# Performance work log

Hardware: AMD Instinct MI355X
Metric: run time of the kernel (lower is better)

Reference implementation:

```python
import jax, jax.numpy as jnp
import numpy as np

N, E, H, S, F = 50000, 800000, 96, 48, 24


def _mlp(x, W1, b1, W2, b2):
    # equinox MLP depth=1: Linear -> relu -> Linear (identity final activation)
    h = jax.nn.relu(x @ W1.T + b1)
    return h @ W2.T + b2


def _segment_softmax(scores, seg, num_segments):
    mx = jax.ops.segment_max(scores, seg, num_segments=num_segments)
    e = jnp.exp(scores - mx[seg])
    s = jax.ops.segment_sum(e, seg, num_segments=num_segments)
    return e / (s[seg] + 1e-9)


def setup_inputs() -> dict:
    key = jax.random.key(0)
    ks = jax.random.split(key, 32)
    def p(i, shape):
        return jax.random.normal(ks[i], shape, dtype=jnp.float32) * 0.05
    in_attn = 2 * H + 2 * S + F   # 312
    w_attn = 2 * H                # 192
    gin = 3 * H                   # 288
    inp = {
        "x": p(0, (N, H)),
        "x_s": p(1, (N, S)),
        "edge_features": p(2, (E, F)),
        "edge_index": jax.random.randint(ks[3], (2, E), 0, N),
        # fwd attention MLP: in_attn -> w_attn -> 1
        "fwd_W1": p(4, (w_attn, in_attn)), "fwd_b1": p(5, (w_attn,)),
        "fwd_W2": p(6, (1, w_attn)), "fwd_b2": p(7, (1,)),
        # rev gate MLP: in_attn -> w_attn -> 1
        "rev_W1": p(8, (w_attn, in_attn)), "rev_b1": p(9, (w_attn,)),
        "rev_W2": p(10, (1, w_attn)), "rev_b2": p(11, (1,)),
        # reset gate MLP: 3H -> 3H -> H
        "reset_W1": p(12, (gin, gin)), "reset_b1": p(13, (gin,)),
        "reset_W2": p(14, (H, gin)), "reset_b2": p(15, (H,)),
        # update gate MLP: 3H -> 3H -> H
        "update_W1": p(16, (gin, gin)), "update_b1": p(17, (gin,)),
        "update_W2": p(18, (H, gin)), "update_b2": p(19, (H,)),
        # candidate MLP: 3H -> 3H -> H
        "cand_W1": p(20, (gin, gin)), "cand_b1": p(21, (gin,)),
        "cand_W2": p(22, (H, gin)), "cand_b2": p(23, (H,)),
    }
    return inp


def reference(x, x_s, edge_features, edge_index,
              fwd_W1, fwd_b1, fwd_W2, fwd_b2,
              rev_W1, rev_b1, rev_W2, rev_b2,
              reset_W1, reset_b1, reset_W2, reset_b2,
              update_W1, update_b1, update_W2, update_b2,
              cand_W1, cand_b1, cand_W2, cand_b2):
    num_nodes = x.shape[0]
    src, dest = edge_index[0], edge_index[1]

    def compute_messages(s, d, W1, b1, W2, b2, use_softmax):
        feat = jnp.concatenate([x[s], x[d], x_s[s], x_s[d], edge_features], axis=-1)
        raw = _mlp(feat, W1, b1, W2, b2)[:, 0]  # [E]
        if use_softmax:
            raw = jax.nn.leaky_relu(raw) / jnp.sqrt(jnp.asarray(x.shape[-1], dtype=x.dtype))
            w = _segment_softmax(raw, d, num_nodes)
        else:
            w = jax.nn.sigmoid(raw)
        agg = jax.ops.segment_sum(x[s] * w[:, None], d, num_segments=num_nodes)
        return agg, w

    fwd_msgs, fwd_w = compute_messages(src, dest, fwd_W1, fwd_b1, fwd_W2, fwd_b2, True)
    rev_msgs, rev_w = compute_messages(dest, src, rev_W1, rev_b1, rev_W2, rev_b2, False)

    messages = jnp.concatenate([fwd_msgs, rev_msgs], axis=-1)  # [N, 2H]
    gate_input = jnp.concatenate([x, messages], axis=-1)        # [N, 3H]
    r_gate = jax.nn.sigmoid(_mlp(gate_input, reset_W1, reset_b1, reset_W2, reset_b2))
    z_gate = jax.nn.sigmoid(_mlp(gate_input, update_W1, update_b1, update_W2, update_b2))
    cand_input = jnp.concatenate([r_gate * x, messages], axis=-1)
    candidate = jnp.tanh(_mlp(cand_input, cand_W1, cand_b1, cand_W2, cand_b2))
    update = (1 - z_gate) * x + z_gate * candidate
    return (update, fwd_w, rev_w, z_gate, r_gate)
```

## Files before the change

### kernel.cpp

```cpp
#include <hip/hip_runtime.h>
#include <math.h>

typedef unsigned short u16;
typedef unsigned int   u32;

#define HDIM 96
#define SDIM 48
#define FDIM 24
#define KA   312
#define WATT 192
#define KG   288

#define AS_E  328
#define KT_A  10
#define KT_G  9
#define NS    296

#define NFRAG (2 * KT_A * 12 * 64)
#define W1F_Q (KT_G * 18 * 64)
#define W2F_Q (KT_G * 6 * 64)
#define NODEF_Q (3 * (W1F_Q + W2F_Q))

typedef __attribute__((ext_vector_type(8))) __bf16 bf16x8;
typedef __attribute__((ext_vector_type(4))) float  f32x4;

__device__ __forceinline__ u16 f2bf(float f) {
  u32 u = __float_as_uint(f);
  u = (u + 0x7FFFu + ((u >> 16) & 1u)) >> 16;
  return (u16)u;
}
__device__ __forceinline__ float bf2f(u16 v) {
  return __uint_as_float((u32)v << 16);
}
__device__ __forceinline__ u32 pack2(float a, float b) {
  return (u32)f2bf(a) | ((u32)f2bf(b) << 16);
}
__device__ __forceinline__ f32x4 mfma_bf16(bf16x8 a, bf16x8 b, f32x4 c) {
  return __builtin_amdgcn_mfma_f32_16x16x32_bf16(a, b, c, 0, 0, 0);
}

__global__ __launch_bounds__(256) void w_prep(
    const float* __restrict__ fW1, const float* __restrict__ rW1,
    uint4* __restrict__ Bfrag)
{
  const int idx = blockIdx.x * 256 + threadIdx.x;
  if (idx >= NFRAG) return;
  const int lane = idx & 63;
  const int frag = idx >> 6;
  const int nt   = frag % 12;
  const int rest = frag / 12;
  const int kt   = rest % KT_A;
  const int mlp  = rest / KT_A;
  const int q = lane >> 4, c = lane & 15;
  const int n  = nt * 16 + c;
  const int p0 = kt * 16 + q * 4;
  const float* W = mlp ? rW1 : fW1;
  u32 v[4];
#pragma unroll
  for (int w = 0; w < 4; ++w) {
    const int p = p0 + w;
    u32 val = 0u;
    if (p < 156) {
      int src = p;
      if (mlp) {
        if (src < 48)       src += 48;
        else if (src < 96)  src -= 48;
        else if (src < 120) src += 24;
        else if (src < 144) src -= 24;
      }
      const float2 wv = *(const float2*)(W + (size_t)n * KA + 2 * src);
      val = pack2(wv.x, wv.y);
    }
    v[w] = val;
  }
  Bfrag[idx] = make_uint4(v[0], v[1], v[2], v[3]);
}

__global__ __launch_bounds__(256) void w_prep_node(
    const float* __restrict__ W, uint4* __restrict__ outf, int NT)
{
  const int nfrag = KT_G * NT * 64;
  const int idx = blockIdx.x * 256 + threadIdx.x;
  if (idx >= nfrag) return;
  const int lane = idx & 63;
  const int frag = idx >> 6;
  const int nt = frag % NT, kt = frag / NT;
  const int q = lane >> 4, c = lane & 15;
  const int n = nt * 16 + c;
  const int k0 = kt * 32 + q * 8;
  u32 v[4];
#pragma unroll
  for (int w = 0; w < 4; ++w) {
    const float2 wv = *(const float2*)(W + (size_t)n * KG + k0 + 2 * w);
    v[w] = pack2(wv.x, wv.y);
  }
  outf[idx] = make_uint4(v[0], v[1], v[2], v[3]);
}

__global__ __launch_bounds__(256) void x_prep(
    const float* __restrict__ x, const float* __restrict__ xs,
    u32* __restrict__ xb, u32* __restrict__ xsb, int N)
{
  const int i = blockIdx.x * 256 + threadIdx.x;
  const int nx = N * 48;
  if (i < nx) {
    const float2 v = ((const float2*)x)[i];
    xb[i] = pack2(v.x, v.y);
  } else if (i < nx + N * 24) {
    const float2 v = ((const float2*)xs)[i - nx];
    xsb[i - nx] = pack2(v.x, v.y);
  }
}

__global__ __launch_bounds__(256, 2) void edge_kernel(
    const u32* __restrict__ xb, const u32* __restrict__ xsb,
    const float* __restrict__ ef, const int* __restrict__ ei,
    const u16* __restrict__ Bfrag,
    const float* __restrict__ fb1, const float* __restrict__ fW2,
    const float* __restrict__ fb2,
    const float* __restrict__ rb1, const float* __restrict__ rW2,
    const float* __restrict__ rb2,
    float* __restrict__ pe, float* __restrict__ out_revw, int N, int E)
{
  __shared__ __align__(16) u16 Alds[64 * AS_E];
  __shared__ float red[4][64];

  const int tid  = threadIdx.x;
  const int wave = tid >> 6, lane = tid & 63;
  const int q = lane >> 4, c = lane & 15;
  const int e0 = blockIdx.x * 64;

  {
    u32* Aw = (u32*)Alds;
    const int el = tid >> 2, sub = tid & 3;
    const int e = min(e0 + el, E - 1);
    int s = ei[e], d = ei[(size_t)E + e];
    s = min(max(s, 0), N - 1); d = min(max(d, 0), N - 1);
    const u32* xs_ = xb  + (size_t)s * 48;
    const u32* xd_ = xb  + (size_t)d * 48;
    const u32* ss_ = xsb + (size_t)s * 24;
    const u32* sd_ = xsb + (size_t)d * 24;
    for (int p = sub; p < 160; p += 4) {
      u32 v = 0u;
      if (p < 48)       v = xs_[p];
      else if (p < 96)  v = xd_[p - 48];
      else if (p < 120) v = ss_[p - 96];
      else if (p < 144) v = sd_[p - 120];
      else if (p < 156) {
        const float2 w = *(const float2*)(ef + (size_t)e * 24 + 2 * (p - 144));
        v = pack2(w.x, w.y);
      }
      Aw[el * (AS_E / 2) + p] = v;
    }
  }
  __syncthreads();

  const bf16x8* __restrict__ Bf = (const bf16x8*)Bfrag;

  for (int mlp = 0; mlp < 2; ++mlp) {
    f32x4 acc[4][3];
#pragma unroll
    for (int m = 0; m < 4; ++m)
      for (int t = 0; t < 3; ++t)
        acc[m][t] = (f32x4){0.f, 0.f, 0.f, 0.f};

#pragma unroll
    for (int kt = 0; kt < KT_A; ++kt) {
      bf16x8 a[4];
#pragma unroll
      for (int m = 0; m < 4; ++m)
        a[m] = *(const bf16x8*)&Alds[(m * 16 + c) * AS_E + kt * 32 + q * 8];
#pragma unroll
      for (int t = 0; t < 3; ++t) {
        const bf16x8 b =
            Bf[(((mlp * KT_A + kt) * 12) + wave * 3 + t) * 64 + lane];
#pragma unroll
        for (int m = 0; m < 4; ++m)
          acc[m][t] = mfma_bf16(a[m], b, acc[m][t]);
      }
    }

    const float* b1p = mlp ? rb1 : fb1;
    const float* W2p = mlp ? rW2 : fW2;
    float p[4][4];
#pragma unroll
    for (int m = 0; m < 4; ++m)
      for (int r = 0; r < 4; ++r) p[m][r] = 0.f;
#pragma unroll
    for (int t = 0; t < 3; ++t) {
      const int n = (wave * 3 + t) * 16 + c;
      const float b1f = b1p[n];
      const float w2f = W2p[n];
#pragma unroll
      for (int m = 0; m < 4; ++m)
        for (int r = 0; r < 4; ++r) {
          float h = acc[m][t][r] + b1f;
          h = h > 0.f ? h : 0.f;
          p[m][r] += h * w2f;
        }
    }
    for (int off = 1; off <= 8; off <<= 1)
#pragma unroll
      for (int m = 0; m < 4; ++m)
        for (int r = 0; r < 4; ++r)
          p[m][r] += __shfl_xor(p[m][r], off, 64);

    __syncthreads();
    if (c == 0) {
#pragma unroll
      for (int m = 0; m < 4; ++m)
        for (int r = 0; r < 4; ++r)
          red[wave][m * 16 + q * 4 + r] = p[m][r];
    }
    __syncthreads();

    if (tid < 64 && e0 + tid < E) {
      float raw = red[0][tid] + red[1][tid] + red[2][tid] + red[3][tid];
      const int e = e0 + tid;
      if (mlp == 0) {
        raw += fb2[0];
        const float lr = raw > 0.f ? raw : 0.01f * raw;
        pe[e] = __expf(lr * 0.10206207261596575f);
      } else {
        raw += rb2[0];
        out_revw[e] = 1.f / (1.f + __expf(-raw));
      }
    }
  }
}

__global__ __launch_bounds__(256) void k_hist(
    const int* __restrict__ ei, int* __restrict__ deg_d,
    int* __restrict__ deg_s, int N, int E)
{
  const int e = blockIdx.x * 256 + threadIdx.x;
  if (e >= E) return;
  const int s = min(max(ei[e], 0), N - 1);
  const int d = min(max(ei[(size_t)E + e], 0), N - 1);
  atomicAdd(&deg_d[d], 1);
  atomicAdd(&deg_s[s], 1);
}

__global__ __launch_bounds__(256) void k_scan1(
    const int* __restrict__ deg_d, const int* __restrict__ deg_s,
    int* __restrict__ start_d, int* __restrict__ start_s,
    int* __restrict__ bsum_d, int* __restrict__ bsum_s, int N)
{
  __shared__ int sh[256];
  const int t = threadIdx.x, i = blockIdx.x * 256 + t;
  {
    const int v = (i < N) ? deg_d[i] : 0;
    sh[t] = v; __syncthreads();
    for (int off = 1; off < 256; off <<= 1) {
      const int u = (t >= off) ? sh[t - off] : 0;
      __syncthreads();
      sh[t] += u;
      __syncthreads();
    }
    if (i < N) start_d[i] = sh[t] - v;
    if (t == 255) bsum_d[blockIdx.x] = sh[255];
    __syncthreads();
  }
  {
    const int v = (i < N) ? deg_s[i] : 0;
    sh[t] = v; __syncthreads();
    for (int off = 1; off < 256; off <<= 1) {
      const int u = (t >= off) ? sh[t - off] : 0;
      __syncthreads();
      sh[t] += u;
      __syncthreads();
    }
    if (i < N) start_s[i] = sh[t] - v;
    if (t == 255) bsum_s[blockIdx.x] = sh[255];
  }
}

__global__ void k_scan2(int* bsum_d, int* bsum_s, int nb) {
  if (threadIdx.x == 0) {
    int r = 0;
    for (int b = 0; b < nb; ++b) { const int t = bsum_d[b]; bsum_d[b] = r; r += t; }
  } else if (threadIdx.x == 1) {
    int r = 0;
    for (int b = 0; b < nb; ++b) { const int t = bsum_s[b]; bsum_s[b] = r; r += t; }
  }
}

__global__ __launch_bounds__(256) void k_scan3(
    int* __restrict__ start_d, int* __restrict__ start_s,
    const int* __restrict__ bsum_d, const int* __restrict__ bsum_s,
    int* __restrict__ pos_d, int* __restrict__ pos_s, int N)
{
  const int i = blockIdx.x * 256 + threadIdx.x;
  if (i >= N) return;
  const int b = i >> 8;
  const int vd = start_d[i] + bsum_d[b]; start_d[i] = vd; pos_d[i] = vd;
  const int vs = start_s[i] + bsum_s[b]; start_s[i] = vs; pos_s[i] = vs;
}

__global__ __launch_bounds__(256) void k_fill(
    const int* __restrict__ ei, int* __restrict__ pos_d,
    int* __restrict__ pos_s, int* __restrict__ eidx_d,
    int* __restrict__ eidx_s, int N, int E)
{
  const int e = blockIdx.x * 256 + threadIdx.x;
  if (e >= E) return;
  const int s = min(max(ei[e], 0), N - 1);
  const int d = min(max(ei[(size_t)E + e], 0), N - 1);
  eidx_d[atomicAdd(&pos_d[d], 1)] = e;
  eidx_s[atomicAdd(&pos_s[s], 1)] = e;
}

template <int DIR>
__global__ __launch_bounds__(256) void k_agg(
    const float* __restrict__ x, const int* __restrict__ ei,
    const float* __restrict__ pe, const float* __restrict__ revw,
    const int* __restrict__ start, const int* __restrict__ endp,
    const int* __restrict__ eidx,
    u16* __restrict__ outm, float* __restrict__ out_fwdw, int N, int E)
{
  const int g = threadIdx.x >> 5;
  const int l = threadIdx.x & 31;
  const int n = blockIdx.x * 8 + g;
  if (n >= N) return;
  const int beg = start[n], end = endp[n];

  float inv = 1.f;
  if (DIR == 0) {
    float sum = 0.f;
    for (int i = beg + l; i < end; i += 32) sum += pe[eidx[i]];
    for (int off = 16; off; off >>= 1) sum += __shfl_xor(sum, off, 32);
    inv = 1.f / (sum + 1e-9f);
    for (int i = beg + l; i < end; i += 32) {
      const int e = eidx[i];
      out_fwdw[e] = pe[e] * inv;
    }
  }

  float a0 = 0.f, a1 = 0.f, a2 = 0.f;
  for (int i = beg; i < end; ++i) {
    const int e = eidx[i];
    const float w = (DIR == 0) ? pe[e] * inv : revw[e];
    const int o = (DIR == 0) ? min(max(ei[e], 0), N - 1)
                             : min(max(ei[(size_t)E + e], 0), N - 1);
    const float* xr = x + (size_t)o * 96;
    a0 += w * xr[l];
    a1 += w * xr[l + 32];
    a2 += w * xr[l + 64];
  }
  u16* orow = outm + (size_t)n * 96;
  orow[l] = f2bf(a0); orow[l + 32] = f2bf(a1); orow[l + 64] = f2bf(a2);
}

__device__ __forceinline__ void node_mlp(
    const u16* __restrict__ Alds, u16* __restrict__ Hlds,
    const bf16x8* __restrict__ W1f, const bf16x8* __restrict__ W2f,
    const float* __restrict__ b1,
    int wave, int lane, int q, int c, int ntc, int ntc2,
    f32x4 (&acc2)[2][2])
{
  f32x4 acc[2][5];
#pragma unroll
  for (int m = 0; m < 2; ++m)
    for (int t = 0; t < 5; ++t) acc[m][t] = (f32x4){0.f, 0.f, 0.f, 0.f};

#pragma unroll
  for (int kt = 0; kt < KT_G; ++kt) {
    const bf16x8 a0 = *(const bf16x8*)&Alds[c * NS + kt * 32 + q * 8];
    const bf16x8 a1 = *(const bf16x8*)&Alds[(16 + c) * NS + kt * 32 + q * 8];
#pragma unroll
    for (int t = 0; t < 5; ++t) {
      if (t < ntc) {
        const int nt = wave + 4 * t;
        const bf16x8 b = W1f[(kt * 18 + nt) * 64 + lane];
        acc[0][t] = mfma_bf16(a0, b, acc[0][t]);
        acc[1][t] = mfma_bf16(a1, b, acc[1][t]);
      }
    }
  }

  __syncthreads();
#pragma unroll
  for (int t = 0; t < 5; ++t) {
    if (t < ntc) {
      const int n = (wave + 4 * t) * 16 + c;
      const float b1f = b1[n];
#pragma unroll
      for (int m = 0; m < 2; ++m)
        for (int r = 0; r < 4; ++r) {
          float h = acc[m][t][r] + b1f;
          h = h > 0.f ? h : 0.f;
          Hlds[(m * 16 + q * 4 + r) * NS + n] = f2bf(h);
        }
    }
  }
  __syncthreads();

#pragma unroll
  for (int m = 0; m < 2; ++m)
    for (int t = 0; t < 2; ++t) acc2[m][t] = (f32x4){0.f, 0.f, 0.f, 0.f};
#pragma unroll
  for (int kt = 0; kt < KT_G; ++kt) {
    const bf16x8 a0 = *(const bf16x8*)&Hlds[c * NS + kt * 32 + q * 8];
    const bf16x8 a1 = *(const bf16x8*)&Hlds[(16 + c) * NS + kt * 32 + q * 8];
#pragma unroll
    for (int t = 0; t < 2; ++t) {
      if (t < ntc2) {
        const int nt = wave + 4 * t;
        const bf16x8 b = W2f[(kt * 6 + nt) * 64 + lane];
        acc2[0][t] = mfma_bf16(a0, b, acc2[0][t]);
        acc2[1][t] = mfma_bf16(a1, b, acc2[1][t]);
      }
    }
  }
}

__global__ __launch_bounds__(256) void node_fused(
    const float* __restrict__ x, const u32* __restrict__ xb,
    const u32* __restrict__ fwdmb, const u32* __restrict__ revmb,
    const uint4* __restrict__ NodeF,
    const float* __restrict__ b1r, const float* __restrict__ b2r,
    const float* __restrict__ b1u, const float* __restrict__ b2u,
    const float* __restrict__ b1c, const float* __restrict__ b2c,
    float* __restrict__ out_r, float* __restrict__ out_z,
    float* __restrict__ out_upd, int N)
{
  __shared__ __align__(16) u16 Alds[32 * NS];
  __shared__ __align__(16) u16 Hlds[32 * NS];

  const int tid = threadIdx.x;
  const int wave = tid >> 6, lane = tid & 63;
  const int q = lane >> 4, c = lane & 15;
  const int n0 = blockIdx.x * 32;
  const int ntc  = (wave < 2) ? 5 : 4;
  const int ntc2 = (wave < 2) ? 2 : 1;

  {
    u32* Aw = (u32*)Alds;
    const int nl = tid >> 3, sub = tid & 7;
    const int node = min(n0 + nl, N - 1);
    const u32* xr = xb    + (size_t)node * 48;
    const u32* fr = fwdmb + (size_t)node * 48;
    const u32* rr = revmb + (size_t)node * 48;
    for (int p = sub; p < 144; p += 8) {
      u32 v;
      if (p < 48)      v = xr[p];
      else if (p < 96) v = fr[p - 48];
      else             v = rr[p - 96];
      Aw[nl * (NS / 2) + p] = v;
    }
  }
  __syncthreads();

  const bf16x8* W1fr = (const bf16x8*)(NodeF);
  const bf16x8* W2fr = (const bf16x8*)(NodeF + W1F_Q);
  const bf16x8* W1fu = (const bf16x8*)(NodeF + W1F_Q + W2F_Q);
  const bf16x8* W2fu = (const bf16x8*)(NodeF + 2 * W1F_Q + W2F_Q);
  const bf16x8* W1fc = (const bf16x8*)(NodeF + 2 * (W1F_Q + W2F_Q));
  const bf16x8* W2fc = (const bf16x8*)(NodeF + 3 * W1F_Q + 2 * W2F_Q);

  f32x4 acc2[2][2];

  node_mlp(Alds, Hlds, W1fr, W2fr, b1r, wave, lane, q, c, ntc, ntc2, acc2);
  float r_reg[2][2][4];
#pragma unroll
  for (int t = 0; t < 2; ++t) {
    if (t < ntc2) {
      const int n2 = (wave + 4 * t) * 16 + c;
      const float b2f = b2r[n2];
#pragma unroll
      for (int m = 0; m < 2; ++m)
        for (int r = 0; r < 4; ++r) {
          const float v = acc2[m][t][r] + b2f;
          const float rv = 1.f / (1.f + __expf(-v));
          r_reg[t][m][r] = rv;
          const int node = n0 + m * 16 + q * 4 + r;
          if (node < N) out_r[(size_t)node * HDIM + n2] = rv;
        }
    }
  }

  node_mlp(Alds, Hlds, W1fu, W2fu, b1u, wave, lane, q, c, ntc, ntc2, acc2);
  float z_reg[2][2][4];
#pragma unroll
  for (int t = 0; t < 2; ++t) {
    if (t < ntc2) {
      const int n2 = (wave + 4 * t) * 16 + c;
      const float b2f = b2u[n2];
#pragma unroll
      for (int m = 0; m < 2; ++m)
        for (int r = 0; r < 4; ++r) {
          const float v = acc2[m][t][r] + b2f;
          const float zv = 1.f / (1.f + __expf(-v));
          z_reg[t][m][r] = zv;
          const int node = n0 + m * 16 + q * 4 + r;
          if (node < N) out_z[(size_t)node * HDIM + n2] = zv;
        }
    }
  }

#pragma unroll
  for (int t = 0; t < 2; ++t) {
    if (t < ntc2) {
      const int n2 = (wave + 4 * t) * 16 + c;
#pragma unroll
      for (int m = 0; m < 2; ++m)
        for (int r = 0; r < 4; ++r) {
          const int row = m * 16 + q * 4 + r;
          const int idx = row * NS + n2;
          Alds[idx] = f2bf(bf2f(Alds[idx]) * r_reg[t][m][r]);
        }
    }
  }
  __syncthreads();

  node_mlp(Alds, Hlds, W1fc, W2fc, b1c, wave, lane, q, c, ntc, ntc2, acc2);
#pragma unroll
  for (int t = 0; t < 2; ++t) {
    if (t < ntc2) {
      const int n2 = (wave + 4 * t) * 16 + c;
      const float b2f = b2c[n2];
#pragma unroll
      for (int m = 0; m < 2; ++m)
        for (int r = 0; r < 4; ++r) {
          const int node = n0 + m * 16 + q * 4 + r;
          if (node < N) {
            const float v = acc2[m][t][r] + b2f;
            const float ct = tanhf(v);
            const float z = z_reg[t][m][r];
            const float xv = x[(size_t)node * HDIM + n2];
            out_upd[(size_t)node * HDIM + n2] = (1.f - z) * xv + z * ct;
          }
        }
    }
  }
}

__global__ void sentinel_kernel(float* out, int n, float val) {
  const int i = blockIdx.x * 256 + threadIdx.x;
  if (i < n) out[i] = val;
}

extern "C" void kernel_launch(void* const* d_in, const int* in_sizes, int n_in,
                              void* d_out, int out_size, void* d_ws, size_t ws_size,
                              hipStream_t stream) {
  const float* x  = (const float*)d_in[0];
  const float* xs = (const float*)d_in[1];
  const float* ef = (const float*)d_in[2];
  const int*   ei = (const int*)d_in[3];

  const int N = in_sizes[0] / HDIM;
  const int E = in_sizes[3] / 2;

  float* out = (float*)d_out;

  const int NB = (N + 255) / 256;

  const bool sizes_ok =
      n_in == 24 && NB <= 1024 &&
      in_sizes[0] == N * HDIM && in_sizes[1] == N * SDIM &&
      in_sizes[2] == E * FDIM && in_sizes[3] == 2 * E &&
      in_sizes[4] == WATT * KA && in_sizes[5] == WATT &&
      in_sizes[6] == WATT && in_sizes[7] == 1 &&
      in_sizes[12] == KG * KG && in_sizes[13] == KG &&
      in_sizes[14] == HDIM * KG && in_sizes[15] == HDIM &&
      out_size == 3 * N * HDIM + 2 * E;
  if (!sizes_ok) {
    sentinel_kernel<<<(out_size + 255) / 256, 256, 0, stream>>>(out, out_size, 777.0f);
    return;
  }

  const size_t eA = ((size_t)E + 3) & ~(size_t)3;
  const size_t needed =
      (eA + (size_t)NFRAG * 4 + (size_t)NODEF_Q * 4 +
       (size_t)N * 48 + (size_t)N * 24 + 2 * (size_t)N * 48 +
       6 * (size_t)N + 2048 + 2 * (size_t)E) * 4;
  if (ws_size < needed) {
    sentinel_kernel<<<(out_size + 255) / 256, 256, 0, stream>>>(out, out_size, 12345.0f);
    return;
  }
  float* pe    = (float*)d_ws;
  uint4* Bfrag = (uint4*)((u32*)d_ws + eA);
  uint4* NodeF = Bfrag + NFRAG;
  u32*   xbw   = (u32*)(NodeF + NODEF_Q);
  u32*   xsbw  = xbw + (size_t)N * 48;
  u32*   fwdmb = xsbw + (size_t)N * 24;
  u32*   revmb = fwdmb + (size_t)N * 48;
  int* deg_d   = (int*)(revmb + (size_t)N * 48);
  int* deg_s   = deg_d + N;
  int* start_d = deg_s + N;
  int* start_s = start_d + N;
  int* pos_d   = start_s + N;
  int* pos_s   = pos_d + N;
  int* bsum_d  = pos_s + N;
  int* bsum_s  = bsum_d + 1024;
  int* eidx_d  = bsum_s + 1024;
  int* eidx_s  = eidx_d + E;

  float* out_update = out;
  float* out_fwdw   = out + (size_t)N * HDIM;
  float* out_revw   = out_fwdw + E;
  float* out_z      = out_revw + E;
  float* out_r      = out_z + (size_t)N * HDIM;

  (void)hipMemsetAsync(deg_d, 0, 2 * (size_t)N * sizeof(int), stream);

  w_prep<<<(NFRAG + 255) / 256, 256, 0, stream>>>(
      (const float*)d_in[4], (const float*)d_in[8], Bfrag);
  const int g1 = (KT_G * 18 * 64 + 255) / 256;
  const int g2 = (KT_G * 6 * 64 + 255) / 256;
  w_prep_node<<<g1, 256, 0, stream>>>((const float*)d_in[12], NodeF, 18);
  w_prep_node<<<g2, 256, 0, stream>>>((const float*)d_in[14], NodeF + W1F_Q, 6);
  w_prep_node<<<g1, 256, 0, stream>>>((const float*)d_in[16],
                                      NodeF + W1F_Q + W2F_Q, 18);
  w_prep_node<<<g2, 256, 0, stream>>>((const float*)d_in[18],
                                      NodeF + 2 * W1F_Q + W2F_Q, 6);
  w_prep_node<<<g1, 256, 0, stream>>>((const float*)d_in[20],
                                      NodeF + 2 * (W1F_Q + W2F_Q), 18);
  w_prep_node<<<g2, 256, 0, stream>>>((const float*)d_in[22],
                                      NodeF + 3 * W1F_Q + 2 * W2F_Q, 6);
  x_prep<<<(N * 72 + 255) / 256, 256, 0, stream>>>(x, xs, xbw, xsbw, N);

  const int eblk = (E + 255) / 256;
  k_hist<<<eblk, 256, 0, stream>>>(ei, deg_d, deg_s, N, E);
  k_scan1<<<NB, 256, 0, stream>>>(deg_d, deg_s, start_d, start_s,
                                  bsum_d, bsum_s, N);
  k_scan2<<<1, 64, 0, stream>>>(bsum_d, bsum_s, NB);
  k_scan3<<<NB, 256, 0, stream>>>(start_d, start_s, bsum_d, bsum_s,
                                  pos_d, pos_s, N);
  k_fill<<<eblk, 256, 0, stream>>>(ei, pos_d, pos_s, eidx_d, eidx_s, N, E);

  edge_kernel<<<(E + 63) / 64, 256, 0, stream>>>(
      xbw, xsbw, ef, ei, (const u16*)Bfrag,
      (const float*)d_in[5], (const float*)d_in[6], (const float*)d_in[7],
      (const float*)d_in[9], (const float*)d_in[10], (const float*)d_in[11],
      pe, out_revw, N, E);

  const int ablk = (N + 7) / 8;
  k_agg<0><<<ablk, 256, 0, stream>>>(x, ei, pe, out_revw, start_d, pos_d,
                                     eidx_d, (u16*)fwdmb, out_fwdw, N, E);
  k_agg<1><<<ablk, 256, 0, stream>>>(x, ei, pe, out_revw, start_s, pos_s,
                                     eidx_s, (u16*)revmb, out_fwdw, N, E);

  const int nblk = (N + 31) / 32;
  node_fused<<<nblk, 256, 0, stream>>>(
      x, xbw, fwdmb, revmb, NodeF,
      (const float*)d_in[13], (const float*)d_in[15],
      (const float*)d_in[17], (const float*)d_in[19],
      (const float*)d_in[21], (const float*)d_in[23],
      out_r, out_z, out_update, N);
}
```

Baseline: 1.164 ms.

## Vectorize gathers to 16-byte loads and double node MLP tile to 64 rows

The edge kernel's feature gather now loads 16-byte vectors per thread, each thread filling a contiguous 10-uint4 chunk of the LDS row instead of strided 4-byte loads. The node kernel goes from 32 to 64 nodes per block, so each weight fragment loaded from global memory feeds four MFMAs instead of two, roughly halving weight traffic per node. It also vectorizes its LDS fill and adds a min-blocks-per-CU hint of 2 to launch bounds. The cost is more accumulator registers and double the LDS per block, which may reduce occupancy, and half as many node blocks.

```diff
diff --git a/kernel.cpp b/kernel.cpp
--- a/kernel.cpp
+++ b/kernel.cpp
@@ -131,27 +131,42 @@
   const int e0 = blockIdx.x * 64;
 
   {
-    u32* Aw = (u32*)Alds;
     const int el = tid >> 2, sub = tid & 3;
     const int e = min(e0 + el, E - 1);
     int s = ei[e], d = ei[(size_t)E + e];
     s = min(max(s, 0), N - 1); d = min(max(d, 0), N - 1);
-    const u32* xs_ = xb  + (size_t)s * 48;
-    const u32* xd_ = xb  + (size_t)d * 48;
-    const u32* ss_ = xsb + (size_t)s * 24;
-    const u32* sd_ = xsb + (size_t)d * 24;
-    for (int p = sub; p < 160; p += 4) {
-      u32 v = 0u;
-      if (p < 48)       v = xs_[p];
-      else if (p < 96)  v = xd_[p - 48];
-      else if (p < 120) v = ss_[p - 96];
-      else if (p < 144) v = sd_[p - 120];
-      else if (p < 156) {
-        const float2 w = *(const float2*)(ef + (size_t)e * 24 + 2 * (p - 144));
-        v = pack2(w.x, w.y);
+    const uint4* xsr = (const uint4*)(xb  + (size_t)s * 48);
+    const uint4* xdr = (const uint4*)(xb  + (size_t)d * 48);
+    const uint4* ssr = (const uint4*)(xsb + (size_t)s * 24);
+    const uint4* sdr = (const uint4*)(xsb + (size_t)d * 24);
+    uint4* Arow = (uint4*)&Alds[el * AS_E];
+    uint4 v[10];
+    if (sub == 0) {
+#pragma unroll
+      for (int i = 0; i < 10; ++i) v[i] = xsr[i];
+    } else if (sub == 1) {
+      v[0] = xsr[10]; v[1] = xsr[11];
+#pragma unroll
+      for (int i = 0; i < 8; ++i) v[2 + i] = xdr[i];
+    } else if (sub == 2) {
+#pragma unroll
+      for (int i = 0; i < 4; ++i) v[i] = xdr[8 + i];
+#pragma unroll
+      for (int i = 0; i < 6; ++i) v[4 + i] = ssr[i];
+    } else {
+#pragma unroll
+      for (int i = 0; i < 6; ++i) v[i] = sdr[i];
+      const float4* efr = (const float4*)(ef + (size_t)e * 24);
+#pragma unroll
+      for (int u = 0; u < 3; ++u) {
+        const float4 a = efr[2 * u], b = efr[2 * u + 1];
+        v[6 + u] = make_uint4(pack2(a.x, a.y), pack2(a.z, a.w),
+                              pack2(b.x, b.y), pack2(b.z, b.w));
       }
-      Aw[el * (AS_E / 2) + p] = v;
-    }
+      v[9] = make_uint4(0u, 0u, 0u, 0u);
+    }
+#pragma unroll
+    for (int i = 0; i < 10; ++i) Arow[sub * 10 + i] = v[i];
   }
   __syncthreads();
 
@@ -356,24 +371,27 @@
     const bf16x8* __restrict__ W1f, const bf16x8* __restrict__ W2f,
     const float* __restrict__ b1,
     int wave, int lane, int q, int c, int ntc, int ntc2,
-    f32x4 (&acc2)[2][2])
-{
-  f32x4 acc[2][5];
-#pragma unroll
-  for (int m = 0; m < 2; ++m)
+    f32x4 (&acc2)[4][2])
+{
+  f32x4 acc[4][5];
+#pragma unroll
+  for (int m = 0; m < 4; ++m)
     for (int t = 0; t < 5; ++t) acc[m][t] = (f32x4){0.f, 0.f, 0.f, 0.f};
 
 #pragma unroll
   for (int kt = 0; kt < KT_G; ++kt) {
-    const bf16x8 a0 = *(const bf16x8*)&Alds[c * NS + kt * 32 + q * 8];
-    const bf16x8 a1 = *(const bf16x8*)&Alds[(16 + c) * NS + kt * 32 + q * 8];
+    bf16x8 a[4];
+#pragma unroll
+    for (int m = 0; m < 4; ++m)
+      a[m] = *(const bf16x8*)&Alds[(m * 16 + c) * NS + kt * 32 + q * 8];
 #pragma unroll
     for (int t = 0; t < 5; ++t) {
       if (t < ntc) {
         const int nt = wave + 4 * t;
         const bf16x8 b = W1f[(kt * 18 + nt) * 64 + lane];
-        acc[0][t] = mfma_bf16(a0, b, acc[0][t]);
-        acc[1][t] = mfma_bf16(a1, b, acc[1][t]);
+#pragma unroll
+        for (int m = 0; m < 4; ++m)
+          acc[m][t] = mfma_bf16(a[m], b, acc[m][t]);
       }
     }
   }
@@ -385,7 +403,7 @@
       const int n = (wave + 4 * t) * 16 + c;
       const float b1f = b1[n];
 #pragma unroll
-      for (int m = 0; m < 2; ++m)
+      for (int m = 0; m < 4; ++m)
         for (int r = 0; r < 4; ++r) {
           float h = acc[m][t][r] + b1f;
           h = h > 0.f ? h : 0.f;
@@ -396,25 +414,28 @@
   __syncthreads();
 
 #pragma unroll
-  for (int m = 0; m < 2; ++m)
+  for (int m = 0; m < 4; ++m)
     for (int t = 0; t < 2; ++t) acc2[m][t] = (f32x4){0.f, 0.f, 0.f, 0.f};
 #pragma unroll
   for (int kt = 0; kt < KT_G; ++kt) {
-    const bf16x8 a0 = *(const bf16x8*)&Hlds[c * NS + kt * 32 + q * 8];
-    const bf16x8 a1 = *(const bf16x8*)&Hlds[(16 + c) * NS + kt * 32 + q * 8];
+    bf16x8 a[4];
+#pragma unroll
+    for (int m = 0; m < 4; ++m)
+      a[m] = *(const bf16x8*)&Hlds[(m * 16 + c) * NS + kt * 32 + q * 8];
 #pragma unroll
     for (int t = 0; t < 2; ++t) {
       if (t < ntc2) {
         const int nt = wave + 4 * t;
         const bf16x8 b = W2f[(kt * 6 + nt) * 64 + lane];
-        acc2[0][t] = mfma_bf16(a0, b, acc2[0][t]);
-        acc2[1][t] = mfma_bf16(a1, b, acc2[1][t]);
+#pragma unroll
+        for (int m = 0; m < 4; ++m)
+          acc2[m][t] = mfma_bf16(a[m], b, acc2[m][t]);
       }
     }
   }
 }
 
-__global__ __launch_bounds__(256) void node_fused(
+__global__ __launch_bounds__(256, 2) void node_fused(
     const float* __restrict__ x, const u32* __restrict__ xb,
     const u32* __restrict__ fwdmb, const u32* __restrict__ revmb,
     const uint4* __restrict__ NodeF,
@@ -424,30 +445,41 @@
     float* __restrict__ out_r, float* __restrict__ out_z,
     float* __restrict__ out_upd, int N)
 {
-  __shared__ __align__(16) u16 Alds[32 * NS];
-  __shared__ __align__(16) u16 Hlds[32 * NS];
+  __shared__ __align__(16) u16 Alds[64 * NS];
+  __shared__ __align__(16) u16 Hlds[64 * NS];
 
   const int tid = threadIdx.x;
   const int wave = tid >> 6, lane = tid & 63;
   const int q = lane >> 4, c = lane & 15;
-  const int n0 = blockIdx.x * 32;
+  const int n0 = blockIdx.x * 64;
   const int ntc  = (wave < 2) ? 5 : 4;
   const int ntc2 = (wave < 2) ? 2 : 1;
 
   {
-    u32* Aw = (u32*)Alds;
-    const int nl = tid >> 3, sub = tid & 7;
+    const int nl = tid >> 2, sub = tid & 3;
     const int node = min(n0 + nl, N - 1);
-    const u32* xr = xb    + (size_t)node * 48;
-    const u32* fr = fwdmb + (size_t)node * 48;
-    const u32* rr = revmb + (size_t)node * 48;
-    for (int p = sub; p < 144; p += 8) {
-      u32 v;
-      if (p < 48)      v = xr[p];
-      else if (p < 96) v = fr[p - 48];
-      else             v = rr[p - 96];
-      Aw[nl * (NS / 2) + p] = v;
-    }
+    const uint4* xr = (const uint4*)(xb    + (size_t)node * 48);
+    const uint4* fr = (const uint4*)(fwdmb + (size_t)node * 48);
+    const uint4* rr = (const uint4*)(revmb + (size_t)node * 48);
+    uint4* Arow = (uint4*)&Alds[nl * NS];
+    uint4 v[9];
+    if (sub == 0) {
+#pragma unroll
+      for (int i = 0; i < 9; ++i) v[i] = xr[i];
+    } else if (sub == 1) {
+      v[0] = xr[9]; v[1] = xr[10]; v[2] = xr[11];
+#pragma unroll
+      for (int i = 0; i < 6; ++i) v[3 + i] = fr[i];
+    } else if (sub == 2) {
+#pragma unroll
+      for (int i = 0; i < 6; ++i) v[i] = fr[6 + i];
+      v[6] = rr[0]; v[7] = rr[1]; v[8] = rr[2];
+    } else {
+#pragma unroll
+      for (int i = 0; i < 9; ++i) v[i] = rr[3 + i];
+    }
+#pragma unroll
+    for (int i = 0; i < 9; ++i) Arow[sub * 9 + i] = v[i];
   }
   __syncthreads();
 
@@ -458,17 +490,17 @@
   const bf16x8* W1fc = (const bf16x8*)(NodeF + 2 * (W1F_Q + W2F_Q));
   const bf16x8* W2fc = (const bf16x8*)(NodeF + 3 * W1F_Q + 2 * W2F_Q);
 
-  f32x4 acc2[2][2];
+  f32x4 acc2[4][2];
 
   node_mlp(Alds, Hlds, W1fr, W2fr, b1r, wave, lane, q, c, ntc, ntc2, acc2);
-  float r_reg[2][2][4];
+  float r_reg[2][4][4];
 #pragma unroll
   for (int t = 0; t < 2; ++t) {
     if (t < ntc2) {
       const int n2 = (wave + 4 * t) * 16 + c;
       const float b2f = b2r[n2];
 #pragma unroll
-      for (int m = 0; m < 2; ++m)
+      for (int m = 0; m < 4; ++m)
         for (int r = 0; r < 4; ++r) {
           const float v = acc2[m][t][r] + b2f;
           const float rv = 1.f / (1.f + __expf(-v));
@@ -480,14 +512,14 @@
   }
 
   node_mlp(Alds, Hlds, W1fu, W2fu, b1u, wave, lane, q, c, ntc, ntc2, acc2);
-  float z_reg[2][2][4];
+  float z_reg[2][4][4];
 #pragma unroll
   for (int t = 0; t < 2; ++t) {
     if (t < ntc2) {
       const int n2 = (wave + 4 * t) * 16 + c;
       const float b2f = b2u[n2];
 #pragma unroll
-      for (int m = 0; m < 2; ++m)
+      for (int m = 0; m < 4; ++m)
         for (int r = 0; r < 4; ++r) {
           const float v = acc2[m][t][r] + b2f;
           const float zv = 1.f / (1.f + __expf(-v));
@@ -503,7 +535,7 @@
     if (t < ntc2) {
       const int n2 = (wave + 4 * t) * 16 + c;
 #pragma unroll
-      for (int m = 0; m < 2; ++m)
+      for (int m = 0; m < 4; ++m)
         for (int r = 0; r < 4; ++r) {
           const int row = m * 16 + q * 4 + r;
           const int idx = row * NS + n2;
@@ -520,7 +552,7 @@
       const int n2 = (wave + 4 * t) * 16 + c;
       const float b2f = b2c[n2];
 #pragma unroll
-      for (int m = 0; m < 2; ++m)
+      for (int m = 0; m < 4; ++m)
         for (int r = 0; r < 4; ++r) {
           const int node = n0 + m * 16 + q * 4 + r;
           if (node < N) {
@@ -641,7 +673,7 @@
   k_agg<1><<<ablk, 256, 0, stream>>>(x, ei, pe, out_revw, start_s, pos_s,
                                      eidx_s, (u16*)revmb, out_fwdw, N, E);
 
-  const int nblk = (N + 31) / 32;
+  const int nblk = (N + 63) / 64;
   node_fused<<<nblk, 256, 0, stream>>>(
       x, xbw, fwdmb, revmb, NodeF,
       (const float*)d_in[13], (const float*)d_in[15],
```

Measured after the change: 1.131 ms. 2.8% less time.
